# Kernel optimization log

Hardware: AMD Instinct MI355X
Metric: run time of the kernel (lower is better)

Reference implementation:

```python
import jax, jax.numpy as jnp
import numpy as np

B, C, LH, LW, HH, HW = 8, 64, 128, 128, 64, 64


def conv3x3(x, w, groups=1):
    # x: NCHW, w: OIHW, stride 1, padding 1 (matches nn.Conv2d(k=3, p=1, bias=False))
    return jax.lax.conv_general_dilated(
        x, w, window_strides=(1, 1), padding=((1, 1), (1, 1)),
        feature_group_count=groups,
        dimension_numbers=('NCHW', 'OIHW', 'NCHW'))


def grid_sample_bilinear(img, grid):
    # F.grid_sample(mode='bilinear', padding_mode='zeros', align_corners=True)
    # img: (N, Cc, H, W); grid: (N, Ho, Wo, 2) with (x, y) in [-1, 1]
    N, Cc, H, W = img.shape
    gx = (grid[..., 0] + 1.0) * 0.5 * (W - 1)
    gy = (grid[..., 1] + 1.0) * 0.5 * (H - 1)
    x0 = jnp.floor(gx)
    y0 = jnp.floor(gy)
    wx1 = gx - x0
    wy1 = gy - y0

    def tap(xi, yi, wgt):
        valid = (xi >= 0) & (xi <= W - 1) & (yi >= 0) & (yi <= H - 1)
        xc = jnp.clip(xi, 0, W - 1).astype(jnp.int32)
        yc = jnp.clip(yi, 0, H - 1).astype(jnp.int32)
        v = jax.vmap(lambda im, y, x: im[:, y, x])(img, yc, xc)  # (N, Cc, Ho, Wo)
        return v * (wgt * valid)[:, None]

    return (tap(x0, y0, (1 - wx1) * (1 - wy1))
            + tap(x0 + 1, y0, wx1 * (1 - wy1))
            + tap(x0, y0 + 1, (1 - wx1) * wy1)
            + tap(x0 + 1, y0 + 1, wx1 * wy1))


def flow_warp(inp, flow, out_h, out_w):
    # base grid in [-1,1] (align_corners=True convention), flow normalized by (out_w, out_h)
    hs = jnp.linspace(-1.0, 1.0, out_h)
    ws = jnp.linspace(-1.0, 1.0, out_w)
    base = jnp.stack(jnp.meshgrid(ws, hs, indexing='xy'), axis=-1)  # (Ho, Wo, 2) as (x, y)
    norm = jnp.array([out_w, out_h], dtype=inp.dtype)
    grid = base[None].astype(inp.dtype) + jnp.transpose(flow, (0, 2, 3, 1)) / norm
    return grid_sample_bilinear(inp, grid)


def setup_inputs() -> dict:
    key = jax.random.key(0)
    k1, k2, k3, k4, k5, k6 = jax.random.split(key, 6)
    return {
        'low_feature': jax.random.normal(k1, (B, C, LH, LW), dtype=jnp.float32),
        'high_feature': jax.random.normal(k2, (B, C, HH, HW), dtype=jnp.float32),
        'w_conv_l': jax.random.normal(k3, (C, 1, 3, 3), dtype=jnp.float32) * 0.1,   # depthwise
        'w_conv_h': jax.random.normal(k4, (C, 1, 3, 3), dtype=jnp.float32) * 0.1,   # depthwise
        'w_flow': jax.random.normal(k5, (4 * C, C, 3, 3), dtype=jnp.float32) * 0.05,
        'w_gate': jax.random.normal(k6, (1, 4, 3, 3), dtype=jnp.float32) * 0.1,
    }


def reference(low_feature, high_feature, w_conv_l, w_conv_h, w_flow, w_gate):
    lb, ln, lh, lw = low_feature.shape
    hb, hn, hh, hw = high_feature.shape
    l_feature = conv3x3(low_feature, w_conv_l, groups=ln)
    h_feature = conv3x3(high_feature, w_conv_h, groups=hn)
    # F.interpolate(mode='bilinear', align_corners=False) == jax.image.resize bilinear
    h_feature = jax.image.resize(h_feature, (hb, hn, lh, lw), method='bilinear')
    flow = conv3x3(l_feature + h_feature, w_flow)          # (B, 4C, lh, lw)
    part = 2 * ln
    flow_h, flow_l = flow[:, :part], flow[:, part:]
    high_r = high_feature.reshape(hb * hn, 1, hh, hw)
    fh = flow_h.reshape(lb * ln, 2, lh, lw)
    high_warp = flow_warp(high_r, fh, lh, lw).reshape(lb, ln, lh, lw)
    low_r = low_feature.reshape(lb * ln, 1, lh, lw)
    fl = flow_l.reshape(lb * ln, 2, lh, lw)
    low_warp = flow_warp(low_r, fl, lh, lw).reshape(lb, ln, lh, lw)
    gate_in = jnp.concatenate([
        h_feature.mean(axis=1, keepdims=True),
        l_feature.mean(axis=1, keepdims=True),
        h_feature.max(axis=1, keepdims=True),
        l_feature.max(axis=1, keepdims=True)], axis=1)     # (B, 4, lh, lw)
    gates = jax.nn.sigmoid(conv3x3(gate_in, w_gate))
    return high_warp * gates + low_warp * (1.0 - gates)
```

## Files before the change

### kernel.cpp

```cpp
#include <hip/hip_runtime.h>
#include <math.h>

#define BB 8
#define CC 64
#define LHH 128
#define LWW 128
#define HHH 64
#define HWW 64

typedef __attribute__((ext_vector_type(8))) short short8v;
typedef __attribute__((ext_vector_type(4))) float f32x4;

typedef struct __attribute__((packed, aligned(4))) {
  float x, y;
} f2u;

#define KCHS 8192
#define SROWB 16640
#define SIMGB (130 * SROWB)
#define KROWB 8448

__device__ __forceinline__ unsigned short f2bf(float f) {
  unsigned u = __float_as_uint(f);
  unsigned r = (u + 0x7fffu + ((u >> 16) & 1u)) >> 16;
  return (unsigned short)r;
}

__global__ __launch_bounds__(256) void dw_high_prep_kernel(
    const float* __restrict__ hf, const float* __restrict__ w,
    float* __restrict__ out, const float* __restrict__ wflow,
    unsigned short* __restrict__ bt) {
  if (blockIdx.x >= 8192) {
    int t = (blockIdx.x - 8192) * 256 + threadIdx.x;
    if (t >= 18 * KCHS) return;
    int kchunk = t / KCHS;
    int rem = t - kchunk * KCHS;
    int oc2 = rem >> 5;
    int kk = rem & 31;
    int dydx = kchunk >> 1;
    int cc = kchunk & 1;
    int ci = cc * 32 + kk;
    int c = oc2 >> 2;
    int j = oc2 & 3;
    int orig = (j >> 1) * 128 + 2 * c + (j & 1);
    bt[t] = f2bf(wflow[(orig * 64 + ci) * 9 + dydx]);
    return;
  }
  int t = blockIdx.x * 256 + threadIdx.x;
  int x = t & 63;
  int y = (t >> 6) & 63;
  int c = (t >> 12) & 63;
  int b = t >> 18;
  const float* img = hf + ((size_t)(b * CC + c)) * (HHH * HWW);
  const float* wc = w + c * 9;
  const int xm = max(x - 1, 0), xp = min(x + 1, 63);
  const int ym = max(y - 1, 0), yp = min(y + 1, 63);
  const float mL = x > 0 ? 1.f : 0.f, mR = x < 63 ? 1.f : 0.f;
  const float mT = y > 0 ? 1.f : 0.f, mB = y < 63 ? 1.f : 0.f;
  const bool xz = (x == 0);
  const int dxp = xp - xm;
  f2u p0 = *(const f2u*)(img + ym * 64 + xm);
  f2u p1 = *(const f2u*)(img + y * 64 + xm);
  f2u p2 = *(const f2u*)(img + yp * 64 + xm);
  float r0p = img[ym * 64 + xm + dxp];
  float r1p = img[y * 64 + xm + dxp];
  float r2p = img[yp * 64 + xm + dxp];
  float r0x = xz ? p0.x : p0.y;
  float r1x = xz ? p1.x : p1.y;
  float r2x = xz ? p2.x : p2.y;
  float t0 = (wc[0] * mL) * p0.x + wc[1] * r0x + (wc[2] * mR) * r0p;
  float t1 = (wc[3] * mL) * p1.x + wc[4] * r1x + (wc[5] * mR) * r1p;
  float t2 = (wc[6] * mL) * p2.x + wc[7] * r2x + (wc[8] * mR) * r2p;
  out[t] = mT * t0 + t1 + mB * t2;
}

__global__ __launch_bounds__(512, 4) void fuse_sum_stats_kernel(
    const float* __restrict__ low, const float* __restrict__ hsm,
    const float* __restrict__ wl, unsigned short* __restrict__ sump,
    float* __restrict__ gate_in) {
  __shared__ unsigned short sumS[128 * 64];
  __shared__ float sh[4][4][128];
  __shared__ float wS[576];

  const int bid = blockIdx.x;
  const int b = bid & 7;
  const int y = bid >> 3;
  const int tid = threadIdx.x;
  const int x = tid & 127;
  const int q = tid >> 7;
  char* sbase = (char*)sump + (size_t)b * SIMGB;

  wS[tid] = wl[tid];
  if (tid < 64) wS[512 + tid] = wl[512 + tid];

  {
    const short8v z = {0, 0, 0, 0, 0, 0, 0, 0};
    if (y == 0) {
      for (int i = tid; i < 2080; i += 512) {
        int row = (i < 1040) ? 0 : 129;
        int o = (i % 1040) * 16;
        *(short8v*)(sbase + (size_t)row * SROWB + o) = z;
      }
    }
    if (tid < 16) {
      int side = tid >> 3;
      int o = (tid & 7) * 16;
      *(short8v*)(sbase + (size_t)(y + 1) * SROWB + side * (129 * 128) + o) = z;
    }
  }
  __syncthreads();

  float sy = 0.5f * y - 0.25f;
  float sx = 0.5f * x - 0.25f;
  float y0f = floorf(sy), x0f = floorf(sx);
  float wy = sy - y0f, wx = sx - x0f;
  int iy0 = (int)y0f, ix0 = (int)x0f;
  int iy0c = max(0, min(HHH - 1, iy0));
  int iy1c = max(0, min(HHH - 1, iy0 + 1));
  float w00 = (1.f - wy) * (1.f - wx), w01 = (1.f - wy) * wx;
  float w10 = wy * (1.f - wx), w11 = wy * wx;
  const int hxb = min(max(ix0, 0), HWW - 2);
  const bool hs0 = (ix0 <= hxb);
  const bool hs1 = (ix0 + 1 <= hxb);

  const int xm = max(x - 1, 0), xp = min(x + 1, 127);
  const int ym = max(y - 1, 0), yp = min(y + 1, 127);
  const float mL = x > 0 ? 1.f : 0.f, mR = x < 127 ? 1.f : 0.f;
  const float mT = y > 0 ? 1.f : 0.f, mB = y < 127 ? 1.f : 0.f;
  const bool xz = (x == 0);

  const unsigned lco = (unsigned)((b * CC + q * 16) * 16384);
  const unsigned hco = (unsigned)((b * CC + q * 16) * 4096);
  const unsigned ro0 = (unsigned)(ym * 128 + xm);
  const unsigned ro1 = (unsigned)(y * 128 + xm);
  const unsigned ro2 = (unsigned)(yp * 128 + xm);
  const unsigned dxp = (unsigned)(xp - xm);
  const unsigned ho0 = (unsigned)(iy0c * 64 + hxb);
  const unsigned ho1 = (unsigned)(iy1c * 64 + hxb);

  float hmean = 0.f, lmean = 0.f;
  float hmax = -3.402823466e+38f, lmax = -3.402823466e+38f;

  unsigned short sv[16];
#pragma unroll 8
  for (int j = 0; j < 16; ++j) {
    const unsigned lo_ = lco + (unsigned)(j * 16384);
    const float* wc = &wS[(q * 16 + j) * 9];
    f2u p0 = *(const f2u*)(low + (lo_ + ro0));
    f2u p1 = *(const f2u*)(low + (lo_ + ro1));
    f2u p2 = *(const f2u*)(low + (lo_ + ro2));
    float r0p = low[lo_ + ro0 + dxp];
    float r1p = low[lo_ + ro1 + dxp];
    float r2p = low[lo_ + ro2 + dxp];
    const unsigned ho_ = hco + (unsigned)(j * 4096);
    f2u q0 = *(const f2u*)(hsm + (ho_ + ho0));
    f2u q1 = *(const f2u*)(hsm + (ho_ + ho1));

    float r0x = xz ? p0.x : p0.y;
    float r1x = xz ? p1.x : p1.y;
    float r2x = xz ? p2.x : p2.y;
    float t0 = (wc[0] * mL) * p0.x + wc[1] * r0x + (wc[2] * mR) * r0p;
    float t1 = (wc[3] * mL) * p1.x + wc[4] * r1x + (wc[5] * mR) * r1p;
    float t2 = (wc[6] * mL) * p2.x + wc[7] * r2x + (wc[8] * mR) * r2p;
    float l = mT * t0 + t1 + mB * t2;

    float h00 = hs0 ? q0.x : q0.y;
    float h01 = hs1 ? q0.x : q0.y;
    float h10 = hs0 ? q1.x : q1.y;
    float h11 = hs1 ? q1.x : q1.y;
    float h = w00 * h00 + w01 * h01 + w10 * h10 + w11 * h11;

    sv[j] = f2bf(l + h);
    hmean += h;
    lmean += l;
    hmax = fmaxf(hmax, h);
    lmax = fmaxf(lmax, l);
  }

  {
    unsigned int pk[8];
#pragma unroll
    for (int j = 0; j < 8; ++j)
      pk[j] = (unsigned)sv[2 * j] | ((unsigned)sv[2 * j + 1] << 16);
    const int u0 = (x * 128 + q * 32) ^ ((x & 7) << 4);
    const int u1 = (x * 128 + q * 32 + 16) ^ ((x & 7) << 4);
    *(short8v*)((char*)sumS + u0) = *(short8v*)&pk[0];
    *(short8v*)((char*)sumS + u1) = *(short8v*)&pk[4];
  }
  sh[0][q][x] = hmean;
  sh[1][q][x] = lmean;
  sh[2][q][x] = hmax;
  sh[3][q][x] = lmax;
  __syncthreads();

  {
    char* dst = sbase + (size_t)(y + 1) * SROWB + 128;
#pragma unroll
    for (int pass = 0; pass < 2; ++pass) {
      int o = (tid + pass * 512) * 16;
      int L = o ^ (((o >> 7) & 7) << 4);
      *(short8v*)(dst + o) = *(const short8v*)((const char*)sumS + L);
    }
  }
  {
    const int s = q;
    float v0 = sh[s][0][x], v1 = sh[s][1][x], v2 = sh[s][2][x],
          v3 = sh[s][3][x];
    float r;
    if (s < 2)
      r = (v0 + v1 + v2 + v3) * (1.0f / CC);
    else
      r = fmaxf(fmaxf(v0, v1), fmaxf(v2, v3));
    gate_in[((size_t)(b * 4 + s)) * 16384 + y * 128 + x] = r;
  }
}

struct BSamp {
  f2u p0, p1;
  float mx0, mx1, my0, my1;
  bool s0, s1;
};

__device__ __forceinline__ BSamp bprep(const float* __restrict__ base,
                                       unsigned coff, int H, int W, float gx,
                                       float gy) {
  BSamp s;
  float x0f = floorf(gx), y0f = floorf(gy);
  float wx1 = gx - x0f, wy1 = gy - y0f;
  int x0 = (int)x0f, y0 = (int)y0f;
  int y1 = y0 + 1;
  s.mx0 = ((unsigned)x0 < (unsigned)W) ? 1.f - wx1 : 0.f;
  s.mx1 = ((unsigned)(x0 + 1) < (unsigned)W) ? wx1 : 0.f;
  s.my0 = ((unsigned)y0 < (unsigned)H) ? 1.f - wy1 : 0.f;
  s.my1 = ((unsigned)y1 < (unsigned)H) ? wy1 : 0.f;
  int xb = min(max(x0, 0), W - 2);
  int y0c = min(max(y0, 0), H - 1);
  int y1c = min(max(y1, 0), H - 1);
  s.p0 = *(const f2u*)(base + (coff + (unsigned)(y0c * W + xb)));
  s.p1 = *(const f2u*)(base + (coff + (unsigned)(y1c * W + xb)));
  s.s0 = (x0 <= xb);
  s.s1 = (x0 + 1 <= xb);
  return s;
}

__device__ __forceinline__ float bfin(const BSamp& s) {
  float v00 = s.s0 ? s.p0.x : s.p0.y;
  float v01 = s.s1 ? s.p0.x : s.p0.y;
  float v10 = s.s0 ? s.p1.x : s.p1.y;
  float v11 = s.s1 ? s.p1.x : s.p1.y;
  return s.my0 * (s.mx0 * v00 + s.mx1 * v01) +
         s.my1 * (s.mx0 * v10 + s.mx1 * v11);
}

__global__ __launch_bounds__(512, 4) void flow_gemm_combine_kernel(
    const unsigned short* __restrict__ sump,
    const unsigned short* __restrict__ bt, const float* __restrict__ low,
    const float* __restrict__ high, const float* __restrict__ gate_in,
    const float* __restrict__ wg, float* __restrict__ out) {
  __shared__ unsigned short ldsU[3 * 4224];
  __shared__ float gateS[64];

  const int bid = blockIdx.x;
  const int b = bid & 7;
  const int y = (bid >> 3) & 127;
  const int xh = bid >> 10;
  const int tid = threadIdx.x;
  const int lane = tid & 63;
  const int wid = tid >> 6;
  const int lr = lane & 15;
  const int lg = lane >> 4;

  {
    const char* src =
        (const char*)sump + (size_t)b * SIMGB + (size_t)y * SROWB + xh * 8192;
    char* dstb = (char*)ldsU;
#pragma unroll
    for (int pass = 0; pass < 3; ++pass) {
      int i = tid + pass * 512;
      int seg = i / 528;
      int wo = (i - seg * 528) * 16;
      int o = seg * KROWB + wo;
      int L = o ^ (((o >> 7) & 7) << 4);
      *(short8v*)(dstb + L) = *(const short8v*)(src + seg * SROWB + wo);
    }
    if (tid < 48) {
      int i = tid + 1536;
      int seg = i / 528;
      int wo = (i - seg * 528) * 16;
      int o = seg * KROWB + wo;
      int L = o ^ (((o >> 7) & 7) << 4);
      *(short8v*)(dstb + L) = *(const short8v*)(src + seg * SROWB + wo);
    }
  }

  if (tid < 64) {
    const int x = xh * 64 + tid;
    const int xm = max(x - 1, 0), xp = min(x + 1, 127);
    const int ym = max(y - 1, 0), yp = min(y + 1, 127);
    const float mL = x > 0 ? 1.f : 0.f, mR = x < 127 ? 1.f : 0.f;
    const float mT = y > 0 ? 1.f : 0.f, mB = y < 127 ? 1.f : 0.f;
    const float* gi = gate_in + (size_t)b * 4 * 16384;
    float acc0 = 0.f;
#pragma unroll
    for (int ic = 0; ic < 4; ++ic) {
      const float* img = gi + ic * 16384;
      const float* wc = wg + ic * 9;
      const float* r0 = img + ym * 128;
      const float* r1 = img + y * 128;
      const float* r2 = img + yp * 128;
      float t0 = (wc[0] * mL) * r0[xm] + wc[1] * r0[x] + (wc[2] * mR) * r0[xp];
      float t1 = (wc[3] * mL) * r1[xm] + wc[4] * r1[x] + (wc[5] * mR) * r1[xp];
      float t2 = (wc[6] * mL) * r2[xm] + wc[7] * r2[x] + (wc[8] * mR) * r2[xp];
      acc0 += mT * t0 + t1 + mB * t2;
    }
    gateS[tid] = 1.0f / (1.0f + expf(-acc0));
  }
  __syncthreads();

  f32x4 acc[4][2];
#pragma unroll
  for (int i = 0; i < 4; ++i)
#pragma unroll
    for (int j = 0; j < 2; ++j) acc[i][j] = (f32x4){0.f, 0.f, 0.f, 0.f};

  const char* rc = (const char*)ldsU;
  const unsigned short* btw = bt + (wid * 32 + lr) * 32 + lg * 8;
  for (int dydx = 0; dydx < 9; ++dydx) {
    const int dy = dydx / 3;
    const int dxl = dydx - dy * 3;
#pragma unroll
    for (int cc = 0; cc < 2; ++cc) {
      const int kchunk = dydx * 2 + cc;
      short8v af[4], bfr[2];
#pragma unroll
      for (int mf = 0; mf < 4; ++mf) {
        const int p = dy * 66 + dxl + mf * 16 + lr;
        const int fa = (p * 128 + cc * 64 + lg * 16) ^ ((p & 7) << 4);
        af[mf] = *(const short8v*)(rc + fa);
      }
#pragma unroll
      for (int nf = 0; nf < 2; ++nf)
        bfr[nf] = *(const short8v*)&btw[kchunk * KCHS + nf * 16 * 32];
#pragma unroll
      for (int mf = 0; mf < 4; ++mf)
#pragma unroll
        for (int nf = 0; nf < 2; ++nf)
          acc[mf][nf] = __builtin_amdgcn_mfma_f32_16x16x32_bf16(
              bfr[nf], af[mf], acc[mf][nf], 0, 0, 0);
    }
  }

  const float* lowb = low + (size_t)b * CC * 16384;
  const float* highb = high + (size_t)b * CC * 4096;
  float* outb = out + (size_t)b * CC * 16384;
  const float by = -1.0f + y * (2.0f / 127.0f);
  const float gyh_b = (by + 1.0f) * 31.5f;
  const float gyl_b = (by + 1.0f) * 63.5f;
  const int xg0 = xh * 64;
  const int c0 = wid * 8 + lg;
  const int c1 = c0 + 4;

#pragma unroll
  for (int mf = 0; mf < 4; ++mf) {
    const int x = xg0 + mf * 16 + lr;
    const float g = gateS[mf * 16 + lr];
    const float bx = -1.0f + x * (2.0f / 127.0f);
    const float gxh_b = (bx + 1.0f) * 31.5f;
    const float gxl_b = (bx + 1.0f) * 63.5f;

    BSamp sh0 = bprep(highb, (unsigned)(c0 * 4096), HHH, HWW,
                      fmaf(acc[mf][0][0], 63.0f / 256.0f, gxh_b),
                      fmaf(acc[mf][0][1], 63.0f / 256.0f, gyh_b));
    BSamp sl0 = bprep(lowb, (unsigned)(c0 * 16384), LHH, LWW,
                      fmaf(acc[mf][0][2], 127.0f / 256.0f, gxl_b),
                      fmaf(acc[mf][0][3], 127.0f / 256.0f, gyl_b));
    BSamp sh1 = bprep(highb, (unsigned)(c1 * 4096), HHH, HWW,
                      fmaf(acc[mf][1][0], 63.0f / 256.0f, gxh_b),
                      fmaf(acc[mf][1][1], 63.0f / 256.0f, gyh_b));
    BSamp sl1 = bprep(lowb, (unsigned)(c1 * 16384), LHH, LWW,
                      fmaf(acc[mf][1][2], 127.0f / 256.0f, gxl_b),
                      fmaf(acc[mf][1][3], 127.0f / 256.0f, gyl_b));

    float h0 = bfin(sh0), l0 = bfin(sl0);
    outb[(unsigned)(c0 * 16384 + y * 128 + x)] = fmaf(g, h0 - l0, l0);
    float h1 = bfin(sh1), l1 = bfin(sl1);
    outb[(unsigned)(c1 * 16384 + y * 128 + x)] = fmaf(g, h1 - l1, l1);
  }
}

extern "C" void kernel_launch(void* const* d_in, const int* in_sizes, int n_in,
                              void* d_out, int out_size, void* d_ws,
                              size_t ws_size, hipStream_t stream) {
  const float* low = (const float*)d_in[0];
  const float* high = (const float*)d_in[1];
  const float* w_conv_l = (const float*)d_in[2];
  const float* w_conv_h = (const float*)d_in[3];
  const float* w_flow = (const float*)d_in[4];
  const float* w_gate = (const float*)d_in[5];
  float* out = (float*)d_out;
  char* ws = (char*)d_ws;

  const size_t OFF_HSMALL = 0;
  const size_t OFF_SUMP = 8388608;
  const size_t OFF_GATEIN = 25694208;
  const size_t OFF_BT = 28315648;

  float* h_small = (float*)(ws + OFF_HSMALL);
  unsigned short* sump = (unsigned short*)(ws + OFF_SUMP);
  float* gate_in = (float*)(ws + OFF_GATEIN);
  unsigned short* bt = (unsigned short*)(ws + OFF_BT);

  dw_high_prep_kernel<<<8192 + 576, 256, 0, stream>>>(high, w_conv_h, h_small,
                                                      w_flow, bt);
  fuse_sum_stats_kernel<<<1024, 512, 0, stream>>>(low, h_small, w_conv_l, sump,
                                                  gate_in);
  flow_gemm_combine_kernel<<<2048, 512, 0, stream>>>(sump, bt, low, high,
                                                     gate_in, w_gate, out);
}
```

Baseline: 104.9 us.

## Process two output rows per block to reuse weight fragments and halo rows

Each block of the flow GEMM/combine kernel now computes two adjacent output rows instead of one, loading four input rows into LDS instead of three and halving the grid. The B (weight) fragments loaded from global memory are reused across both rows' MFMAs, and the shared halo rows cut LDS staging traffic per output row. The cost is double the accumulator registers, which may lower occupancy under launch_bounds(512,4), and half as many blocks for 256 CUs.

```diff
diff --git a/kernel.cpp b/kernel.cpp
--- a/kernel.cpp
+++ b/kernel.cpp
@@ -257,13 +257,14 @@
     const unsigned short* __restrict__ bt, const float* __restrict__ low,
     const float* __restrict__ high, const float* __restrict__ gate_in,
     const float* __restrict__ wg, float* __restrict__ out) {
-  __shared__ unsigned short ldsU[3 * 4224];
-  __shared__ float gateS[64];
+  __shared__ unsigned short ldsU[4 * 4224];
+  __shared__ float gateS[128];
 
   const int bid = blockIdx.x;
   const int b = bid & 7;
-  const int y = (bid >> 3) & 127;
-  const int xh = bid >> 10;
+  const int ypair = (bid >> 3) & 63;
+  const int xh = bid >> 9;
+  const int y0 = ypair * 2;
   const int tid = threadIdx.x;
   const int lane = tid & 63;
   const int wid = tid >> 6;
@@ -272,10 +273,10 @@
 
   {
     const char* src =
-        (const char*)sump + (size_t)b * SIMGB + (size_t)y * SROWB + xh * 8192;
+        (const char*)sump + (size_t)b * SIMGB + (size_t)y0 * SROWB + xh * 8192;
     char* dstb = (char*)ldsU;
 #pragma unroll
-    for (int pass = 0; pass < 3; ++pass) {
+    for (int pass = 0; pass < 4; ++pass) {
       int i = tid + pass * 512;
       int seg = i / 528;
       int wo = (i - seg * 528) * 16;
@@ -283,8 +284,8 @@
       int L = o ^ (((o >> 7) & 7) << 4);
       *(short8v*)(dstb + L) = *(const short8v*)(src + seg * SROWB + wo);
     }
-    if (tid < 48) {
-      int i = tid + 1536;
+    if (tid < 64) {
+      int i = tid + 2048;
       int seg = i / 528;
       int wo = (i - seg * 528) * 16;
       int o = seg * KROWB + wo;
@@ -293,8 +294,10 @@
     }
   }
 
-  if (tid < 64) {
-    const int x = xh * 64 + tid;
+  if (tid < 128) {
+    const int r = tid >> 6;
+    const int x = xh * 64 + (tid & 63);
+    const int y = y0 + r;
     const int xm = max(x - 1, 0), xp = min(x + 1, 127);
     const int ym = max(y - 1, 0), yp = min(y + 1, 127);
     const float mL = x > 0 ? 1.f : 0.f, mR = x < 127 ? 1.f : 0.f;
@@ -317,11 +320,14 @@
   }
   __syncthreads();
 
-  f32x4 acc[4][2];
+  f32x4 acc0[4][2], acc1[4][2];
 #pragma unroll
   for (int i = 0; i < 4; ++i)
 #pragma unroll
-    for (int j = 0; j < 2; ++j) acc[i][j] = (f32x4){0.f, 0.f, 0.f, 0.f};
+    for (int j = 0; j < 2; ++j) {
+      acc0[i][j] = (f32x4){0.f, 0.f, 0.f, 0.f};
+      acc1[i][j] = (f32x4){0.f, 0.f, 0.f, 0.f};
+    }
 
   const char* rc = (const char*)ldsU;
   const unsigned short* btw = bt + (wid * 32 + lr) * 32 + lg * 8;
@@ -331,61 +337,72 @@
 #pragma unroll
     for (int cc = 0; cc < 2; ++cc) {
       const int kchunk = dydx * 2 + cc;
-      short8v af[4], bfr[2];
+      short8v af0[4], af1[4], bfr[2];
+#pragma unroll
+      for (int nf = 0; nf < 2; ++nf)
+        bfr[nf] = *(const short8v*)&btw[kchunk * KCHS + nf * 16 * 32];
 #pragma unroll
       for (int mf = 0; mf < 4; ++mf) {
         const int p = dy * 66 + dxl + mf * 16 + lr;
         const int fa = (p * 128 + cc * 64 + lg * 16) ^ ((p & 7) << 4);
-        af[mf] = *(const short8v*)(rc + fa);
+        af0[mf] = *(const short8v*)(rc + fa);
+        const int p1 = p + 66;
+        const int fb = (p1 * 128 + cc * 64 + lg * 16) ^ ((p1 & 7) << 4);
+        af1[mf] = *(const short8v*)(rc + fb);
       }
 #pragma unroll
-      for (int nf = 0; nf < 2; ++nf)
-        bfr[nf] = *(const short8v*)&btw[kchunk * KCHS + nf * 16 * 32];
-#pragma unroll
       for (int mf = 0; mf < 4; ++mf)
 #pragma unroll
-        for (int nf = 0; nf < 2; ++nf)
-          acc[mf][nf] = __builtin_amdgcn_mfma_f32_16x16x32_bf16(
-              bfr[nf], af[mf], acc[mf][nf], 0, 0, 0);
+        for (int nf = 0; nf < 2; ++nf) {
+          acc0[mf][nf] = __builtin_amdgcn_mfma_f32_16x16x32_bf16(
+              bfr[nf], af0[mf], acc0[mf][nf], 0, 0, 0);
+          acc1[mf][nf] = __builtin_amdgcn_mfma_f32_16x16x32_bf16(
+              bfr[nf], af1[mf], acc1[mf][nf], 0, 0, 0);
+        }
     }
   }
 
   const float* lowb = low + (size_t)b * CC * 16384;
   const float* highb = high + (size_t)b * CC * 4096;
   float* outb = out + (size_t)b * CC * 16384;
-  const float by = -1.0f + y * (2.0f / 127.0f);
-  const float gyh_b = (by + 1.0f) * 31.5f;
-  const float gyl_b = (by + 1.0f) * 63.5f;
   const int xg0 = xh * 64;
   const int c0 = wid * 8 + lg;
   const int c1 = c0 + 4;
 
-#pragma unroll
-  for (int mf = 0; mf < 4; ++mf) {
-    const int x = xg0 + mf * 16 + lr;
-    const float g = gateS[mf * 16 + lr];
-    const float bx = -1.0f + x * (2.0f / 127.0f);
-    const float gxh_b = (bx + 1.0f) * 31.5f;
-    const float gxl_b = (bx + 1.0f) * 63.5f;
-
-    BSamp sh0 = bprep(highb, (unsigned)(c0 * 4096), HHH, HWW,
-                      fmaf(acc[mf][0][0], 63.0f / 256.0f, gxh_b),
-                      fmaf(acc[mf][0][1], 63.0f / 256.0f, gyh_b));
-    BSamp sl0 = bprep(lowb, (unsigned)(c0 * 16384), LHH, LWW,
-                      fmaf(acc[mf][0][2], 127.0f / 256.0f, gxl_b),
-                      fmaf(acc[mf][0][3], 127.0f / 256.0f, gyl_b));
-    BSamp sh1 = bprep(highb, (unsigned)(c1 * 4096), HHH, HWW,
-                      fmaf(acc[mf][1][0], 63.0f / 256.0f, gxh_b),
-                      fmaf(acc[mf][1][1], 63.0f / 256.0f, gyh_b));
-    BSamp sl1 = bprep(lowb, (unsigned)(c1 * 16384), LHH, LWW,
-                      fmaf(acc[mf][1][2], 127.0f / 256.0f, gxl_b),
-                      fmaf(acc[mf][1][3], 127.0f / 256.0f, gyl_b));
-
-    float h0 = bfin(sh0), l0 = bfin(sl0);
-    outb[(unsigned)(c0 * 16384 + y * 128 + x)] = fmaf(g, h0 - l0, l0);
-    float h1 = bfin(sh1), l1 = bfin(sl1);
-    outb[(unsigned)(c1 * 16384 + y * 128 + x)] = fmaf(g, h1 - l1, l1);
-  }
+  auto combine_row = [&](const f32x4(&ac)[4][2], int y, int gbase) {
+    const float by = -1.0f + y * (2.0f / 127.0f);
+    const float gyh_b = (by + 1.0f) * 31.5f;
+    const float gyl_b = (by + 1.0f) * 63.5f;
+#pragma unroll
+    for (int mf = 0; mf < 4; ++mf) {
+      const int x = xg0 + mf * 16 + lr;
+      const float g = gateS[gbase + mf * 16 + lr];
+      const float bx = -1.0f + x * (2.0f / 127.0f);
+      const float gxh_b = (bx + 1.0f) * 31.5f;
+      const float gxl_b = (bx + 1.0f) * 63.5f;
+
+      BSamp sh0 = bprep(highb, (unsigned)(c0 * 4096), HHH, HWW,
+                        fmaf(ac[mf][0][0], 63.0f / 256.0f, gxh_b),
+                        fmaf(ac[mf][0][1], 63.0f / 256.0f, gyh_b));
+      BSamp sl0 = bprep(lowb, (unsigned)(c0 * 16384), LHH, LWW,
+                        fmaf(ac[mf][0][2], 127.0f / 256.0f, gxl_b),
+                        fmaf(ac[mf][0][3], 127.0f / 256.0f, gyl_b));
+      BSamp sh1 = bprep(highb, (unsigned)(c1 * 4096), HHH, HWW,
+                        fmaf(ac[mf][1][0], 63.0f / 256.0f, gxh_b),
+                        fmaf(ac[mf][1][1], 63.0f / 256.0f, gyh_b));
+      BSamp sl1 = bprep(lowb, (unsigned)(c1 * 16384), LHH, LWW,
+                        fmaf(ac[mf][1][2], 127.0f / 256.0f, gxl_b),
+                        fmaf(ac[mf][1][3], 127.0f / 256.0f, gyl_b));
+
+      float h0 = bfin(sh0), l0 = bfin(sl0);
+      outb[(unsigned)(c0 * 16384 + y * 128 + x)] = fmaf(g, h0 - l0, l0);
+      float h1 = bfin(sh1), l1 = bfin(sl1);
+      outb[(unsigned)(c1 * 16384 + y * 128 + x)] = fmaf(g, h1 - l1, l1);
+    }
+  };
+
+  combine_row(acc0, y0, 0);
+  combine_row(acc1, y0 + 1, 64);
 }
 
 extern "C" void kernel_launch(void* const* d_in, const int* in_sizes, int n_in,
@@ -414,6 +431,6 @@
                                                       w_flow, bt);
   fuse_sum_stats_kernel<<<1024, 512, 0, stream>>>(low, h_small, w_conv_l, sump,
                                                   gate_in);
-  flow_gemm_combine_kernel<<<2048, 512, 0, stream>>>(sump, bt, low, high,
+  flow_gemm_combine_kernel<<<1024, 512, 0, stream>>>(sump, bt, low, high,
                                                      gate_in, w_gate, out);
 }
```

Result: faster. 95.98 us (-8.5%).
